# Kernel optimization log

Hardware: AMD Instinct MI355X
Metric: run time of the kernel (lower is better)

The kernel has to match this reference:

```python
import jax, jax.numpy as jnp
import numpy as np

B, C_COMB, HW_IN, HW_FEAT, N_POS, D_PROJ, OUT_HW = 32, 448, 32, 64, 4096, 100, 256


def setup_inputs() -> dict:
    key = jax.random.key(0)
    k1, k2, k3, k4 = jax.random.split(key, 4)
    return {
        "combined": jax.random.normal(k1, (B, C_COMB, HW_IN, HW_IN), dtype=jnp.float32),
        "proj_w": jax.random.normal(k2, (D_PROJ, C_COMB), dtype=jnp.float32),
        "proj_b": jnp.zeros((D_PROJ,), dtype=jnp.float32),
        "mean": jax.random.normal(k3, (D_PROJ, N_POS), dtype=jnp.float32),
        "inv_covariance": jax.random.normal(k4, (N_POS, D_PROJ, D_PROJ), dtype=jnp.float32),
        "norm_min": jnp.zeros((), dtype=jnp.float32),
        "norm_max": jnp.ones((), dtype=jnp.float32),
    }


def reference(combined, proj_w, proj_b, mean, inv_covariance, norm_min, norm_max):
    b = combined.shape[0]
    # F.interpolate(..., size=(64,64), mode='bilinear', align_corners=False)
    feats = jax.image.resize(combined, (b, C_COMB, HW_FEAT, HW_FEAT), method="bilinear")
    # permute to NHWC and flatten spatial -> [B, 4096, 448]
    feats = feats.transpose(0, 2, 3, 1).reshape(b, N_POS, C_COMB)
    # nn.Linear(channels, 100) -> [B, 4096, 100]
    feats = jnp.einsum("bnc,dc->bnd", feats, proj_w) + proj_b
    # per-pixel Mahalanobis quadratic form: diff_n^T @ Sigma_n^{-1} @ diff_n
    diff = feats - mean.T[None]                                  # [B, 4096, 100]
    dist = jnp.einsum("bnc,ncd,bnd->bn", diff, inv_covariance, diff)  # [B, 4096]
    anomaly_map = dist.reshape(b, 1, HW_FEAT, HW_FEAT)
    anomaly_map = (anomaly_map - norm_min) / (norm_max - norm_min + 1e-8)
    anomaly_map = jax.image.resize(anomaly_map, (b, 1, OUT_HW, OUT_HW), method="bilinear")
    return anomaly_map
```

## Files before the change

### kernel.cpp

```cpp
#include <hip/hip_runtime.h>

#define B_      32
#define C_COMB  448
#define N_POS_  4096
#define D_      100

typedef __attribute__((ext_vector_type(8))) short bf16x8;
typedef __attribute__((ext_vector_type(4))) float f32x4;

__device__ __forceinline__ unsigned short f2bf(float f) {
    unsigned u = __builtin_bit_cast(unsigned, f);
    u += 0x7FFFu + ((u >> 16) & 1u);
    return (unsigned short)(u >> 16);
}
__device__ __forceinline__ unsigned pack2bf(float a, float b) {
    return (unsigned)f2bf(a) | ((unsigned)f2bf(b) << 16);
}
__device__ __forceinline__ float bf2f(unsigned short h) {
    return __builtin_bit_cast(float, (unsigned)h << 16);
}
__device__ __forceinline__ float4 bf4_to_f4(uint2 u) {
    float4 r;
    r.x = __builtin_bit_cast(float, u.x << 16);
    r.y = __builtin_bit_cast(float, u.x & 0xffff0000u);
    r.z = __builtin_bit_cast(float, u.y << 16);
    r.w = __builtin_bit_cast(float, u.y & 0xffff0000u);
    return r;
}

__global__ __launch_bounds__(256) void k_prep(const float* __restrict__ W,
                                              unsigned short* __restrict__ Wb,
                                              const float* __restrict__ mean,
                                              float* __restrict__ meanT) {
    int i = blockIdx.x * 256 + threadIdx.x;
    if (i < 11200) {
        float4 v = ((const float4*)W)[i];
        ((uint2*)Wb)[i] = make_uint2(pack2bf(v.x, v.y), pack2bf(v.z, v.w));
    }
    if (i < D_ * N_POS_) {
        int d = i >> 12;
        int n = i & 4095;
        meanT[n * D_ + d] = mean[i];
    }
}

__global__ __launch_bounds__(256) void k_proj(const float* __restrict__ comb,
                                              const unsigned short* __restrict__ Wb,
                                              const float* __restrict__ bias,
                                              unsigned short* __restrict__ p32b) {
    __shared__ float Tf[32 * 65];
    __shared__ unsigned short Ws[D_ * 40];

    const int pt = blockIdx.x, b = blockIdx.y;
    const int t = threadIdx.x;
    const int lane = t & 63, w = t >> 6;
    const int c = lane & 15, q = lane >> 4;

    f32x4 acc[7];
#pragma unroll
    for (int mt = 0; mt < 7; mt++) acc[mt] = (f32x4){0.f, 0.f, 0.f, 0.f};

    const float4* comb4 = (const float4*)comb;

    for (int kt = 0; kt < 14; kt++) {
        __syncthreads();
#pragma unroll
        for (int k = 0; k < 2; k++) {
            int e4 = t + 256 * k;
            int cc = e4 >> 4, p4 = e4 & 15;
            float4 v = comb4[((size_t)b * C_COMB + kt * 32 + cc) * 256 + pt * 16 + p4];
            Tf[cc * 65 + p4 * 4 + 0] = v.x;
            Tf[cc * 65 + p4 * 4 + 1] = v.y;
            Tf[cc * 65 + p4 * 4 + 2] = v.z;
            Tf[cc * 65 + p4 * 4 + 3] = v.w;
        }
#pragma unroll
        for (int k = 0; k < 4; k++) {
            int e = t + 256 * k;
            if (e < 800) {
                int d = e >> 3, c4 = e & 7;
                *(uint2*)(Ws + d * 40 + c4 * 4) =
                    *(const uint2*)(Wb + d * C_COMB + kt * 32 + c4 * 4);
            }
        }
        __syncthreads();

        bf16x8 bfrag;
#pragma unroll
        for (int j = 0; j < 8; j++) {
            bfrag[j] = (short)f2bf(Tf[(q * 8 + j) * 65 + w * 16 + c]);
        }
#pragma unroll
        for (int mt = 0; mt < 7; mt++) {
            int r = mt * 16 + c;
            bf16x8 afrag;
            if (r < D_) afrag = *(const bf16x8*)(Ws + r * 40 + q * 8);
            else        afrag = (bf16x8){0,0,0,0,0,0,0,0};
            acc[mt] = __builtin_amdgcn_mfma_f32_16x16x32_bf16(afrag, bfrag, acc[mt], 0, 0, 0);
        }
    }

    const int pos = pt * 64 + w * 16 + c;
#pragma unroll
    for (int mt = 0; mt < 7; mt++) {
        int d0 = mt * 16 + q * 4;
        if (d0 < D_) {
            f32x4 a = acc[mt];
            float o0 = a[0] + bias[d0 + 0];
            float o1 = a[1] + bias[d0 + 1];
            float o2 = a[2] + bias[d0 + 2];
            float o3 = a[3] + bias[d0 + 3];
            *(uint2*)(p32b + ((size_t)pos * B_ + b) * D_ + d0) =
                make_uint2(pack2bf(o0, o1), pack2bf(o2, o3));
        }
    }
}

__global__ __launch_bounds__(256) void k_mahal(const unsigned short* __restrict__ p32b,
                                               const float* __restrict__ meanT,
                                               const float* __restrict__ icov,
                                               float* __restrict__ gdist) {
    __shared__ unsigned short Mb[D_ * 104];
    __shared__ unsigned short dTb[B_ * 104];
    __shared__ float part[64];

    const int n = blockIdx.x;
    const int t = threadIdx.x;
    const int lane = t & 63, w = t >> 6;
    const int c = lane & 15, q = lane >> 4;

    if (t < 100) *(uint2*)(Mb + t * 104 + 100) = make_uint2(0u, 0u);
    if (t >= 128 && t < 160) *(uint2*)(dTb + (t - 128) * 104 + 100) = make_uint2(0u, 0u);

    const float4* gM4 = (const float4*)(icov + (size_t)n * (D_ * D_));
#pragma unroll
    for (int k = 0; k < 10; k++) {
        int e4 = t + 256 * k;
        if (e4 < 2500) {
            float4 v = gM4[e4];
            int r = e4 / 25, c4 = e4 - r * 25;
            *(uint2*)(Mb + r * 104 + c4 * 4) =
                make_uint2(pack2bf(v.x, v.y), pack2bf(v.z, v.w));
        }
    }

    const int y = n >> 6, x = n & 63;
    float sy = 0.5f * y - 0.25f, sx = 0.5f * x - 0.25f;
    float y0f = floorf(sy), x0f = floorf(sx);
    float fy = sy - y0f, fx = sx - x0f;
    int iy0 = max((int)y0f, 0), iy1 = min((int)y0f + 1, 31);
    int ix0 = max((int)x0f, 0), ix1 = min((int)x0f + 1, 31);
    const float w00 = (1.f - fy) * (1.f - fx), w01 = (1.f - fy) * fx;
    const float w10 = fy * (1.f - fx),         w11 = fy * fx;
    const unsigned short* s00 = p32b + (size_t)(iy0 * 32 + ix0) * 3200;
    const unsigned short* s01 = p32b + (size_t)(iy0 * 32 + ix1) * 3200;
    const unsigned short* s10 = p32b + (size_t)(iy1 * 32 + ix0) * 3200;
    const unsigned short* s11 = p32b + (size_t)(iy1 * 32 + ix1) * 3200;

    const float4* mt4 = (const float4*)meanT + n * 25;
#pragma unroll
    for (int k = 0; k < 4; k++) {
        int e4 = t + 256 * k;
        if (e4 < 800) {
            int b  = e4 / 25;
            int d4 = e4 - b * 25;
            float4 f00 = bf4_to_f4(*(const uint2*)(s00 + e4 * 4));
            float4 f01 = bf4_to_f4(*(const uint2*)(s01 + e4 * 4));
            float4 f10 = bf4_to_f4(*(const uint2*)(s10 + e4 * 4));
            float4 f11 = bf4_to_f4(*(const uint2*)(s11 + e4 * 4));
            float4 m = mt4[d4];
            float vx = w00 * f00.x + w01 * f01.x + w10 * f10.x + w11 * f11.x - m.x;
            float vy = w00 * f00.y + w01 * f01.y + w10 * f10.y + w11 * f11.y - m.y;
            float vz = w00 * f00.z + w01 * f01.z + w10 * f10.z + w11 * f11.z - m.z;
            float vw = w00 * f00.w + w01 * f01.w + w10 * f10.w + w11 * f11.w - m.w;
            *(uint2*)(dTb + b * 104 + d4 * 4) =
                make_uint2(pack2bf(vx, vy), pack2bf(vz, vw));
        }
    }
    __syncthreads();

    const int g = w & 1, h = w >> 1;
    const int bb = g * 16 + c;
    const int mt0 = h * 4;
    f32x4 acc[4];
#pragma unroll
    for (int mi = 0; mi < 4; mi++) acc[mi] = (f32x4){0.f, 0.f, 0.f, 0.f};

#pragma unroll
    for (int kt = 0; kt < 4; kt++) {
        int k0 = kt * 32 + q * 8;
        bf16x8 bfrag;
        if (k0 < 104) bfrag = *(const bf16x8*)(dTb + bb * 104 + k0);
        else          bfrag = (bf16x8){0,0,0,0,0,0,0,0};
#pragma unroll
        for (int mi = 0; mi < 4; mi++) {
            int mt = mt0 + mi;
            if (mt >= 7) continue;
            int r = mt * 16 + c;
            bf16x8 afrag;
            if (r < D_ && k0 < 104) afrag = *(const bf16x8*)(Mb + r * 104 + k0);
            else                    afrag = (bf16x8){0,0,0,0,0,0,0,0};
            acc[mi] = __builtin_amdgcn_mfma_f32_16x16x32_bf16(afrag, bfrag, acc[mi], 0, 0, 0);
        }
    }

    float dist = 0.f;
#pragma unroll
    for (int mi = 0; mi < 4; mi++) {
        int mt = mt0 + mi;
        if (mt >= 7) continue;
#pragma unroll
        for (int reg = 0; reg < 4; reg++) {
            int r = mt * 16 + q * 4 + reg;
            if (r < D_) dist += acc[mi][reg] * bf2f(dTb[bb * 104 + r]);
        }
    }
    dist += __shfl_xor(dist, 16);
    dist += __shfl_xor(dist, 32);
    if (q == 0) part[w * 16 + c] = dist;
    __syncthreads();
    if (t < 32) {
        int gg = t >> 4, cc = t & 15;
        float s = part[gg * 16 + cc] + part[(gg + 2) * 16 + cc];
        gdist[t * N_POS_ + n] = s;
    }
}

__global__ __launch_bounds__(256) void k_upsample(const float* __restrict__ gdist,
                                                  const float* __restrict__ nminp,
                                                  const float* __restrict__ nmaxp,
                                                  float* __restrict__ out) {
    int gid = blockIdx.x * 256 + threadIdx.x;
    int b   = gid >> 16;
    int rem = gid & 65535;
    int Y = rem >> 8, X = rem & 255;
    float sy = 0.25f * Y - 0.375f, sx = 0.25f * X - 0.375f;
    float y0f = floorf(sy), x0f = floorf(sx);
    float fy = sy - y0f, fx = sx - x0f;
    int iy0 = max((int)y0f, 0), iy1 = min((int)y0f + 1, 63);
    int ix0 = max((int)x0f, 0), ix1 = min((int)x0f + 1, 63);
    const float* g = gdist + b * N_POS_;
    float v00 = g[iy0 * 64 + ix0], v01 = g[iy0 * 64 + ix1];
    float v10 = g[iy1 * 64 + ix0], v11 = g[iy1 * 64 + ix1];
    float v = (1.f - fy) * ((1.f - fx) * v00 + fx * v01)
            +        fy  * ((1.f - fx) * v10 + fx * v11);
    float nmin = nminp[0], nmax = nmaxp[0];
    float scale = 1.0f / (nmax - nmin + 1e-8f);
    out[gid] = (v - nmin) * scale;
}

extern "C" void kernel_launch(void* const* d_in, const int* in_sizes, int n_in,
                              void* d_out, int out_size, void* d_ws, size_t ws_size,
                              hipStream_t stream) {
    const float* comb = (const float*)d_in[0];
    const float* W    = (const float*)d_in[1];
    const float* bias = (const float*)d_in[2];
    const float* mean = (const float*)d_in[3];
    const float* icov = (const float*)d_in[4];
    const float* nmin = (const float*)d_in[5];
    const float* nmax = (const float*)d_in[6];
    float* out = (float*)d_out;

    char* ws = (char*)d_ws;
    unsigned short* p32b  = (unsigned short*)(ws);
    float*          meanT = (float*)(ws + 6553600);
    unsigned short* Wb    = (unsigned short*)(ws + 8192000);
    float*          gdist = (float*)(ws + 8281600);

    k_prep    <<<1600, 256, 0, stream>>>(W, Wb, mean, meanT);
    k_proj    <<<dim3(16, 32), 256, 0, stream>>>(comb, Wb, bias, p32b);
    k_mahal   <<<4096, 256, 0, stream>>>(p32b, meanT, icov, gdist);
    k_upsample<<<8192, 256, 0, stream>>>(gdist, nmin, nmax, out);
}
```

Before: 317.1 us.

## Load covariance directly into MFMA fragments and drop mean transpose pass

k_mahal no longer stages the per-position 100x100 inverse covariance through shared memory. Each wave now reads its rows straight from global memory into registers, converts them to bf16, and feeds a single 32x32x16 MFMA chain instead of several 16x16x32 tiles. The mean is read per block with a strided gather into shared memory, which removes the separate transpose work in k_prep and its workspace buffer. The cost is strided, uncoalesced global reads for mean and per-lane row reads of icov, in exchange for less LDS traffic, fewer barriers and one less large prep pass.

New measurement: 310.0 us. -2.2%, faster.

```diff
diff --git a/kernel.cpp b/kernel.cpp
--- a/kernel.cpp
+++ b/kernel.cpp
@@ -5,8 +5,9 @@
 #define N_POS_  4096
 #define D_      100
 
-typedef __attribute__((ext_vector_type(8))) short bf16x8;
-typedef __attribute__((ext_vector_type(4))) float f32x4;
+typedef __attribute__((ext_vector_type(8)))  short bf16x8;
+typedef __attribute__((ext_vector_type(4)))  float f32x4;
+typedef __attribute__((ext_vector_type(16))) float f32x16;
 
 __device__ __forceinline__ unsigned short f2bf(float f) {
     unsigned u = __builtin_bit_cast(unsigned, f);
@@ -27,20 +28,21 @@
     r.w = __builtin_bit_cast(float, u.y & 0xffff0000u);
     return r;
 }
+__device__ __forceinline__ bf16x8 pack8bf(float4 lo, float4 hi) {
+    bf16x8 r;
+    r[0] = (short)f2bf(lo.x); r[1] = (short)f2bf(lo.y);
+    r[2] = (short)f2bf(lo.z); r[3] = (short)f2bf(lo.w);
+    r[4] = (short)f2bf(hi.x); r[5] = (short)f2bf(hi.y);
+    r[6] = (short)f2bf(hi.z); r[7] = (short)f2bf(hi.w);
+    return r;
+}
 
 __global__ __launch_bounds__(256) void k_prep(const float* __restrict__ W,
-                                              unsigned short* __restrict__ Wb,
-                                              const float* __restrict__ mean,
-                                              float* __restrict__ meanT) {
+                                              unsigned short* __restrict__ Wb) {
     int i = blockIdx.x * 256 + threadIdx.x;
     if (i < 11200) {
         float4 v = ((const float4*)W)[i];
         ((uint2*)Wb)[i] = make_uint2(pack2bf(v.x, v.y), pack2bf(v.z, v.w));
-    }
-    if (i < D_ * N_POS_) {
-        int d = i >> 12;
-        int n = i & 4095;
-        meanT[n * D_ + d] = mean[i];
     }
 }
 
@@ -117,32 +119,21 @@
 }
 
 __global__ __launch_bounds__(256) void k_mahal(const unsigned short* __restrict__ p32b,
-                                               const float* __restrict__ meanT,
+                                               const float* __restrict__ mean,
                                                const float* __restrict__ icov,
                                                float* __restrict__ gdist) {
-    __shared__ unsigned short Mb[D_ * 104];
     __shared__ unsigned short dTb[B_ * 104];
-    __shared__ float part[64];
+    __shared__ float meanL[112];
+    __shared__ float part[128];
 
     const int n = blockIdx.x;
     const int t = threadIdx.x;
     const int lane = t & 63, w = t >> 6;
-    const int c = lane & 15, q = lane >> 4;
-
-    if (t < 100) *(uint2*)(Mb + t * 104 + 100) = make_uint2(0u, 0u);
+    const int half = lane >> 5;
+    const int l31  = lane & 31;
+
+    if (t < 100) meanL[t] = mean[t * N_POS_ + n];
     if (t >= 128 && t < 160) *(uint2*)(dTb + (t - 128) * 104 + 100) = make_uint2(0u, 0u);
-
-    const float4* gM4 = (const float4*)(icov + (size_t)n * (D_ * D_));
-#pragma unroll
-    for (int k = 0; k < 10; k++) {
-        int e4 = t + 256 * k;
-        if (e4 < 2500) {
-            float4 v = gM4[e4];
-            int r = e4 / 25, c4 = e4 - r * 25;
-            *(uint2*)(Mb + r * 104 + c4 * 4) =
-                make_uint2(pack2bf(v.x, v.y), pack2bf(v.z, v.w));
-        }
-    }
 
     const int y = n >> 6, x = n & 63;
     float sy = 0.5f * y - 0.25f, sx = 0.5f * x - 0.25f;
@@ -157,7 +148,8 @@
     const unsigned short* s10 = p32b + (size_t)(iy1 * 32 + ix0) * 3200;
     const unsigned short* s11 = p32b + (size_t)(iy1 * 32 + ix1) * 3200;
 
-    const float4* mt4 = (const float4*)meanT + n * 25;
+    __syncthreads();
+
 #pragma unroll
     for (int k = 0; k < 4; k++) {
         int e4 = t + 256 * k;
@@ -168,7 +160,7 @@
             float4 f01 = bf4_to_f4(*(const uint2*)(s01 + e4 * 4));
             float4 f10 = bf4_to_f4(*(const uint2*)(s10 + e4 * 4));
             float4 f11 = bf4_to_f4(*(const uint2*)(s11 + e4 * 4));
-            float4 m = mt4[d4];
+            float4 m = *(const float4*)(meanL + d4 * 4);
             float vx = w00 * f00.x + w01 * f01.x + w10 * f10.x + w11 * f11.x - m.x;
             float vy = w00 * f00.y + w01 * f01.y + w10 * f10.y + w11 * f11.y - m.y;
             float vz = w00 * f00.z + w01 * f01.z + w10 * f10.z + w11 * f11.z - m.z;
@@ -179,49 +171,41 @@
     }
     __syncthreads();
 
-    const int g = w & 1, h = w >> 1;
-    const int bb = g * 16 + c;
-    const int mt0 = h * 4;
-    f32x4 acc[4];
-#pragma unroll
-    for (int mi = 0; mi < 4; mi++) acc[mi] = (f32x4){0.f, 0.f, 0.f, 0.f};
-
-#pragma unroll
-    for (int kt = 0; kt < 4; kt++) {
-        int k0 = kt * 32 + q * 8;
+    const int r = 32 * w + l31;
+    const bool rv = (r < D_);
+    const float* Mrow = icov + (size_t)n * (D_ * D_) + (size_t)r * D_;
+
+    f32x16 acc = {0.f,0.f,0.f,0.f,0.f,0.f,0.f,0.f,0.f,0.f,0.f,0.f,0.f,0.f,0.f,0.f};
+#pragma unroll
+    for (int kt = 0; kt < 7; kt++) {
+        int k0 = kt * 16 + half * 8;
+        bf16x8 afrag;
+        if (rv && k0 < D_) {
+            float4 lo = *(const float4*)(Mrow + k0);
+            float4 hi;
+            if (k0 + 4 < D_) hi = *(const float4*)(Mrow + k0 + 4);
+            else             hi = (float4){0.f, 0.f, 0.f, 0.f};
+            afrag = pack8bf(lo, hi);
+        } else {
+            afrag = (bf16x8){0,0,0,0,0,0,0,0};
+        }
         bf16x8 bfrag;
-        if (k0 < 104) bfrag = *(const bf16x8*)(dTb + bb * 104 + k0);
-        else          bfrag = (bf16x8){0,0,0,0,0,0,0,0};
-#pragma unroll
-        for (int mi = 0; mi < 4; mi++) {
-            int mt = mt0 + mi;
-            if (mt >= 7) continue;
-            int r = mt * 16 + c;
-            bf16x8 afrag;
-            if (r < D_ && k0 < 104) afrag = *(const bf16x8*)(Mb + r * 104 + k0);
-            else                    afrag = (bf16x8){0,0,0,0,0,0,0,0};
-            acc[mi] = __builtin_amdgcn_mfma_f32_16x16x32_bf16(afrag, bfrag, acc[mi], 0, 0, 0);
-        }
+        if (k0 < D_) bfrag = *(const bf16x8*)(dTb + l31 * 104 + k0);
+        else         bfrag = (bf16x8){0,0,0,0,0,0,0,0};
+        acc = __builtin_amdgcn_mfma_f32_32x32x16_bf16(afrag, bfrag, acc, 0, 0, 0);
     }
 
     float dist = 0.f;
 #pragma unroll
-    for (int mi = 0; mi < 4; mi++) {
-        int mt = mt0 + mi;
-        if (mt >= 7) continue;
-#pragma unroll
-        for (int reg = 0; reg < 4; reg++) {
-            int r = mt * 16 + q * 4 + reg;
-            if (r < D_) dist += acc[mi][reg] * bf2f(dTb[bb * 104 + r]);
-        }
-    }
-    dist += __shfl_xor(dist, 16);
+    for (int reg = 0; reg < 16; reg++) {
+        int rr = 32 * w + (reg & 3) + 8 * (reg >> 2) + 4 * half;
+        if (rr < D_) dist += acc[reg] * bf2f(dTb[l31 * 104 + rr]);
+    }
     dist += __shfl_xor(dist, 32);
-    if (q == 0) part[w * 16 + c] = dist;
+    if (half == 0) part[w * 32 + l31] = dist;
     __syncthreads();
     if (t < 32) {
-        int gg = t >> 4, cc = t & 15;
-        float s = part[gg * 16 + cc] + part[(gg + 2) * 16 + cc];
+        float s = part[t] + part[32 + t] + part[64 + t] + part[96 + t];
         gdist[t * N_POS_ + n] = s;
     }
 }
@@ -263,12 +247,11 @@
 
     char* ws = (char*)d_ws;
     unsigned short* p32b  = (unsigned short*)(ws);
-    float*          meanT = (float*)(ws + 6553600);
-    unsigned short* Wb    = (unsigned short*)(ws + 8192000);
-    float*          gdist = (float*)(ws + 8281600);
-
-    k_prep    <<<1600, 256, 0, stream>>>(W, Wb, mean, meanT);
+    unsigned short* Wb    = (unsigned short*)(ws + 6553600);
+    float*          gdist = (float*)(ws + 6643200);
+
+    k_prep    <<<44, 256, 0, stream>>>(W, Wb);
     k_proj    <<<dim3(16, 32), 256, 0, stream>>>(comb, Wb, bias, p32b);
-    k_mahal   <<<4096, 256, 0, stream>>>(p32b, meanT, icov, gdist);
+    k_mahal   <<<4096, 256, 0, stream>>>(p32b, mean, icov, gdist);
     k_upsample<<<8192, 256, 0, stream>>>(gdist, nmin, nmax, out);
 }
```
